# Kernel optimization log

Measured on AMD Instinct MI355X. Metric: run time of the kernel, lower is better.

## Reference

```python
import jax, jax.numpy as jnp
import numpy as np
import math


def _build_lookup(S):
    # Vectorized port of build_hierarchical_index_lookup_table (static, numpy).
    L = int(math.log2(S))
    total = 2 * S - 1
    max_valid = total - 2  # root is never a neighbor
    idx = np.full((S, L), -1, dtype=np.int32)
    cmask = np.zeros((S, L), dtype=bool)
    n = np.arange(S, dtype=np.int64)
    for lvl in range(L):
        if lvl == 0:
            nn = n ^ 1
            pair = n
        else:
            pair = n // 2 + S
            nn = pair ^ 1
        valid = nn <= max_valid
        idx[:, lvl] = np.where(valid, nn.astype(np.int32), idx[:, lvl])
        cmask[:, lvl] = np.where(valid, (pair < nn) & valid, cmask[:, lvl])
        n = nn
    return jnp.asarray(idx), jnp.asarray(cmask)


def _tree_kv(k, v, levels, scale):
    # Build parent nodes bottom-up. Parent K is the mean of its two children;
    # parent V is refined by the fused parent-self attention (build_parent_nodes):
    # 3-way softmax over [self, child0, child1] with eps 1e-9 in the denominator.
    K_parts, V_parts = [k], [v]
    Kc, Vc = k, v
    for _ in range(levels):
        Kc0, Kc1 = Kc[:, 0::2], Kc[:, 1::2]
        Vc0, Vc1 = Vc[:, 0::2], Vc[:, 1::2]
        Kp = 0.5 * (Kc0 + Kc1)
        Vp = 0.5 * (Vc0 + Vc1)
        s_self = jnp.einsum('bphd,bphd->bph', Kp, Kp) * scale
        s0 = jnp.einsum('bphd,bphd->bph', Kp, Kc0) * scale
        s1 = jnp.einsum('bphd,bphd->bph', Kp, Kc1) * scale
        m = jnp.maximum(s_self, jnp.maximum(s0, s1))
        e_self = jnp.exp(s_self - m)
        e0 = jnp.exp(s0 - m)
        e1 = jnp.exp(s1 - m)
        denom = e_self + e0 + e1 + 1e-9
        Vp = (e_self[..., None] * Vp + e0[..., None] * Vc0 + e1[..., None] * Vc1) / denom[..., None]
        K_parts.append(Kp)
        V_parts.append(Vp)
        Kc, Vc = Kp, Vp
    # Full tree: leaves first, then each parent level -> [B, 2S-1, H, D]
    return jnp.concatenate(K_parts, axis=1), jnp.concatenate(V_parts, axis=1)


def setup_inputs() -> dict:
    key = jax.random.key(0)
    kq, kk, kv = jax.random.split(key, 3)
    B, S, H, D = 4, 4096, 8, 64
    q = jax.random.normal(kq, (B, S, H, D), dtype=jnp.float32)
    k = jax.random.normal(kk, (B, S, H, D), dtype=jnp.float32)
    v = jax.random.normal(kv, (B, S, H, D), dtype=jnp.float32)
    return {'q': q, 'k': k, 'v': v}


def reference(q, k, v):
    B, S, H, D = q.shape
    L = int(math.log2(S))
    scale = 1.0 / math.sqrt(D)
    idx, cmask = _build_lookup(S)          # [S, L] int32, [S, L] bool
    Kf, Vf = _tree_kv(k, v, L, scale)      # [B, 2S-1, H, D]
    kc = Kf[:, idx]                        # [B, S, L, H, D] tree-indexed gather
    vc = Vf[:, idx]
    s_self = jnp.einsum('bshd,bshd->bsh', q, k) * scale
    s_cross = jnp.einsum('bshd,bslhd->bshl', q, kc) * scale
    s_cross = jnp.where(cmask[None, :, None, :], -jnp.inf, s_cross)
    m = jnp.maximum(s_self, jnp.max(s_cross, axis=-1))  # online-softmax max
    e_self = jnp.exp(s_self - m)
    e_cross = jnp.exp(s_cross - m[..., None])
    denom = e_self + jnp.sum(e_cross, axis=-1)
    out = (e_self[..., None] * v + jnp.einsum('bshl,bslhd->bshd', e_cross, vc)) / denom[..., None]
    return out
```

## Files before the change

### kernel.cpp

```cpp
#include <hip/hip_runtime.h>


#define S 4096
#define H 8
#define D 64
#define B 4
#define NINT 4094
#define NBH 32
#define SCALE 0.125f

__device__ inline float red16(float x) {
    x += __shfl_xor(x, 1);
    x += __shfl_xor(x, 2);
    x += __shfl_xor(x, 4);
    x += __shfl_xor(x, 8);
    return x;
}

__device__ inline float dot4(const float4 a, const float4 b) {
    return a.x * b.x + a.y * b.y + a.z * b.z + a.w * b.w;
}

__device__ inline void combine(const float4 k0, const float4 k1,
                               const float4 v0, const float4 v1,
                               float4& kp, float4& vp) {
    kp.x = 0.5f * (k0.x + k1.x);
    kp.y = 0.5f * (k0.y + k1.y);
    kp.z = 0.5f * (k0.z + k1.z);
    kp.w = 0.5f * (k0.w + k1.w);
    float pss = red16(dot4(kp, kp)) * SCALE;
    float p0  = red16(dot4(kp, k0)) * SCALE;
    float p1  = red16(dot4(kp, k1)) * SCALE;
    float m  = fmaxf(pss, fmaxf(p0, p1));
    float es = __expf(pss - m), e0 = __expf(p0 - m), e1 = __expf(p1 - m);
    float inv = 1.0f / (es + e0 + e1 + 1e-9f);
    float h = 0.5f * es;
    vp.x = ((h + e0) * v0.x + (h + e1) * v1.x) * inv;
    vp.y = ((h + e0) * v0.y + (h + e1) * v1.y) * inv;
    vp.z = ((h + e0) * v0.z + (h + e1) * v1.z) * inv;
    vp.w = ((h + e0) * v0.w + (h + e1) * v1.w) * inv;
}

__global__ __launch_bounds__(256) void tree_chunk(
    const float* __restrict__ k, const float* __restrict__ v,
    float* __restrict__ kt, float* __restrict__ vt)
{
    __shared__ float lk[127 * 64];
    __shared__ float lv[127 * 64];
    const int t = threadIdx.x;
    const int sub = t & 15;
    const int pg = t >> 4;
    const int blk = blockIdx.x;
    const int c = blk & 31;
    const int bh = blk >> 5;
    const int b = bh >> 3, h = bh & 7;

    for (int j = pg; j < 64; j += 16) {
        int s0 = c * 128 + 2 * j;
        size_t a0 = ((((size_t)b * S + s0) * H + h) * D) + sub * 4;
        float4 k0 = *(const float4*)(k + a0);
        float4 k1 = *(const float4*)(k + a0 + H * D);
        float4 v0 = *(const float4*)(v + a0);
        float4 v1 = *(const float4*)(v + a0 + H * D);
        float4 kp, vp;
        combine(k0, k1, v0, v1, kp, vp);
        *(float4*)(lk + j * 64 + sub * 4) = kp;
        *(float4*)(lv + j * 64 + sub * 4) = vp;
        size_t g = ((size_t)bh * NINT + c * 64 + j) * 64 + sub * 4;
        *(float4*)(kt + g) = kp;
        *(float4*)(vt + g) = vp;
    }
    __syncthreads();

    int coff = 0;
    for (int l = 2; l <= 7; ++l) {
        int np = 128 >> l;
        int poff = coff + (128 >> (l - 1));
        int goff = S - (S >> (l - 1));
        for (int j = pg; j < np; j += 16) {
            float4 k0 = *(const float4*)(lk + (coff + 2 * j) * 64 + sub * 4);
            float4 k1 = *(const float4*)(lk + (coff + 2 * j + 1) * 64 + sub * 4);
            float4 v0 = *(const float4*)(lv + (coff + 2 * j) * 64 + sub * 4);
            float4 v1 = *(const float4*)(lv + (coff + 2 * j + 1) * 64 + sub * 4);
            float4 kp, vp;
            combine(k0, k1, v0, v1, kp, vp);
            *(float4*)(lk + (poff + j) * 64 + sub * 4) = kp;
            *(float4*)(lv + (poff + j) * 64 + sub * 4) = vp;
            size_t g = ((size_t)bh * NINT + goff + c * np + j) * 64 + sub * 4;
            *(float4*)(kt + g) = kp;
            *(float4*)(vt + g) = vp;
        }
        __syncthreads();
        coff = poff;
    }
}

__global__ __launch_bounds__(256) void tree_top(
    float* __restrict__ kt, float* __restrict__ vt)
{
    __shared__ float lk[62 * 64];
    __shared__ float lv[62 * 64];
    const int t = threadIdx.x;
    const int sub = t & 15;
    const int pg = t >> 4;
    const int bh = blockIdx.x;

    for (int i = t; i < 512; i += 256) {
        size_t g = ((size_t)bh * NINT + (S - (S >> 6))) * 64 + i * 4;
        *(float4*)(lk + i * 4) = *(const float4*)(kt + g);
        *(float4*)(lv + i * 4) = *(const float4*)(vt + g);
    }
    __syncthreads();

    int coff = 0, cn = 32;
    for (int l = 8; l <= 11; ++l) {
        int np = cn >> 1;
        int poff = coff + cn;
        int goff = S - (S >> (l - 1));
        if (pg < np) {
            int j = pg;
            float4 k0 = *(const float4*)(lk + (coff + 2 * j) * 64 + sub * 4);
            float4 k1 = *(const float4*)(lk + (coff + 2 * j + 1) * 64 + sub * 4);
            float4 v0 = *(const float4*)(lv + (coff + 2 * j) * 64 + sub * 4);
            float4 v1 = *(const float4*)(lv + (coff + 2 * j + 1) * 64 + sub * 4);
            float4 kp, vp;
            combine(k0, k1, v0, v1, kp, vp);
            *(float4*)(lk + (poff + j) * 64 + sub * 4) = kp;
            *(float4*)(lv + (poff + j) * 64 + sub * 4) = vp;
            size_t g = ((size_t)bh * NINT + goff + j) * 64 + sub * 4;
            *(float4*)(kt + g) = kp;
            *(float4*)(vt + g) = vp;
        }
        __syncthreads();
        coff = poff; cn = np;
    }
}

__global__ __launch_bounds__(256) void attn(
    const float* __restrict__ q, const float* __restrict__ k,
    const float* __restrict__ v,
    const float* __restrict__ kt, const float* __restrict__ vt,
    float* __restrict__ out)
{
    int t = blockIdx.x * 256 + threadIdx.x;
    int lane = t & 63;
    int sub = lane & 15;
    int qi = lane >> 4;
    int w = t >> 6;
    int hg = w & 1;
    int s = (w >> 1) & (S - 1);
    int b = w >> 13;
    int h = hg * 4 + qi;
    int bh = b * 8 + h;
    size_t qa = ((((size_t)b * S + s) * H + h) * D) + sub * 4;

    float4 q4 = *(const float4*)(q + qa);
    float4 k4 = *(const float4*)(k + qa);
    float4 v4 = *(const float4*)(v + qa);
    float ss = red16(dot4(q4, k4)) * SCALE;

    float m = ss, denom = 1.0f;
    float4 acc = v4;
    size_t tb = (size_t)bh * NINT;

#pragma unroll
    for (int l = 0; l < 12; ++l) {
        if ((s >> l) & 1) {
            float4 kc, vc;
            if (l == 0) {
                kc = *(const float4*)(k + qa - H * D);
                vc = *(const float4*)(v + qa - H * D);
            } else {
                int node = (S - (S >> (l - 1))) + ((s >> l) ^ 1);
                size_t a = (tb + node) * 64 + sub * 4;
                kc = *(const float4*)(kt + a);
                vc = *(const float4*)(vt + a);
            }
            float sc = red16(dot4(q4, kc)) * SCALE;
            float nm = fmaxf(m, sc);
            float c1 = __expf(m - nm);
            float e  = __expf(sc - nm);
            denom = denom * c1 + e;
            acc.x = acc.x * c1 + e * vc.x;
            acc.y = acc.y * c1 + e * vc.y;
            acc.z = acc.z * c1 + e * vc.z;
            acc.w = acc.w * c1 + e * vc.w;
            m = nm;
        }
    }
    float inv = 1.0f / denom;
    float4 o;
    o.x = acc.x * inv; o.y = acc.y * inv; o.z = acc.z * inv; o.w = acc.w * inv;
    *(float4*)(out + qa) = o;
}

extern "C" void kernel_launch(void* const* d_in, const int* in_sizes, int n_in,
                              void* d_out, int out_size, void* d_ws, size_t ws_size,
                              hipStream_t stream) {
    const float* q = (const float*)d_in[0];
    const float* k = (const float*)d_in[1];
    const float* v = (const float*)d_in[2];
    float* outp = (float*)d_out;
    float* kt = (float*)d_ws;
    float* vt = kt + (size_t)NBH * NINT * D;

    hipLaunchKernelGGL(tree_chunk, dim3(NBH * 32), dim3(256), 0, stream,
                       k, v, kt, vt);
    hipLaunchKernelGGL(tree_top, dim3(NBH), dim3(256), 0, stream, kt, vt);
    hipLaunchKernelGGL(attn, dim3((B * S * 2 * 64) / 256), dim3(256), 0, stream,
                       q, k, v, kt, vt, outp);
}
```

Measured before the change: 181.2 us.

## Batch tree-node loads in attention and rebalance tree build across kernels

```diff
diff --git a/kernel.cpp b/kernel.cpp
--- a/kernel.cpp
+++ b/kernel.cpp
@@ -45,18 +45,20 @@
     const float* __restrict__ k, const float* __restrict__ v,
     float* __restrict__ kt, float* __restrict__ vt)
 {
-    __shared__ float lk[127 * 64];
-    __shared__ float lv[127 * 64];
+    __shared__ float lkA[32 * 64], lvA[32 * 64];
+    __shared__ float lkB[16 * 64], lvB[16 * 64];
     const int t = threadIdx.x;
     const int sub = t & 15;
     const int pg = t >> 4;
     const int blk = blockIdx.x;
-    const int c = blk & 31;
-    const int bh = blk >> 5;
+    const int c = blk & 63;
+    const int bh = blk >> 6;
     const int b = bh >> 3, h = bh & 7;
 
-    for (int j = pg; j < 64; j += 16) {
-        int s0 = c * 128 + 2 * j;
+#pragma unroll
+    for (int r = 0; r < 2; ++r) {
+        int j = pg + r * 16;
+        int s0 = c * 64 + 2 * j;
         size_t a0 = ((((size_t)b * S + s0) * H + h) * D) + sub * 4;
         float4 k0 = *(const float4*)(k + a0);
         float4 k1 = *(const float4*)(k + a0 + H * D);
@@ -64,75 +66,85 @@
         float4 v1 = *(const float4*)(v + a0 + H * D);
         float4 kp, vp;
         combine(k0, k1, v0, v1, kp, vp);
-        *(float4*)(lk + j * 64 + sub * 4) = kp;
-        *(float4*)(lv + j * 64 + sub * 4) = vp;
-        size_t g = ((size_t)bh * NINT + c * 64 + j) * 64 + sub * 4;
+        *(float4*)(lkA + j * 64 + sub * 4) = kp;
+        *(float4*)(lvA + j * 64 + sub * 4) = vp;
+        size_t g = ((size_t)bh * NINT + c * 32 + j) * 64 + sub * 4;
         *(float4*)(kt + g) = kp;
         *(float4*)(vt + g) = vp;
     }
     __syncthreads();
 
-    int coff = 0;
-    for (int l = 2; l <= 7; ++l) {
-        int np = 128 >> l;
-        int poff = coff + (128 >> (l - 1));
+    float *sk = lkA, *sv = lvA, *dk = lkB, *dv = lvB;
+#pragma unroll
+    for (int l = 2; l <= 6; ++l) {
+        int np = 64 >> l;
         int goff = S - (S >> (l - 1));
-        for (int j = pg; j < np; j += 16) {
-            float4 k0 = *(const float4*)(lk + (coff + 2 * j) * 64 + sub * 4);
-            float4 k1 = *(const float4*)(lk + (coff + 2 * j + 1) * 64 + sub * 4);
-            float4 v0 = *(const float4*)(lv + (coff + 2 * j) * 64 + sub * 4);
-            float4 v1 = *(const float4*)(lv + (coff + 2 * j + 1) * 64 + sub * 4);
+        if (pg < np) {
+            int j = pg;
+            float4 k0 = *(const float4*)(sk + (2 * j) * 64 + sub * 4);
+            float4 k1 = *(const float4*)(sk + (2 * j + 1) * 64 + sub * 4);
+            float4 v0 = *(const float4*)(sv + (2 * j) * 64 + sub * 4);
+            float4 v1 = *(const float4*)(sv + (2 * j + 1) * 64 + sub * 4);
             float4 kp, vp;
             combine(k0, k1, v0, v1, kp, vp);
-            *(float4*)(lk + (poff + j) * 64 + sub * 4) = kp;
-            *(float4*)(lv + (poff + j) * 64 + sub * 4) = vp;
+            if (l < 6) {
+                *(float4*)(dk + j * 64 + sub * 4) = kp;
+                *(float4*)(dv + j * 64 + sub * 4) = vp;
+            }
             size_t g = ((size_t)bh * NINT + goff + c * np + j) * 64 + sub * 4;
             *(float4*)(kt + g) = kp;
             *(float4*)(vt + g) = vp;
         }
         __syncthreads();
-        coff = poff;
+        float* tp;
+        tp = sk; sk = dk; dk = tp;
+        tp = sv; sv = dv; dv = tp;
     }
 }
 
 __global__ __launch_bounds__(256) void tree_top(
     float* __restrict__ kt, float* __restrict__ vt)
 {
-    __shared__ float lk[62 * 64];
-    __shared__ float lv[62 * 64];
+    __shared__ float lkA[64 * 64], lvA[64 * 64];
+    __shared__ float lkB[32 * 64], lvB[32 * 64];
     const int t = threadIdx.x;
     const int sub = t & 15;
     const int pg = t >> 4;
     const int bh = blockIdx.x;
 
-    for (int i = t; i < 512; i += 256) {
-        size_t g = ((size_t)bh * NINT + (S - (S >> 6))) * 64 + i * 4;
-        *(float4*)(lk + i * 4) = *(const float4*)(kt + g);
-        *(float4*)(lv + i * 4) = *(const float4*)(vt + g);
+    for (int i = t; i < 1024; i += 256) {
+        size_t g = ((size_t)bh * NINT + 3968) * 64 + i * 4;
+        *(float4*)(lkA + i * 4) = *(const float4*)(kt + g);
+        *(float4*)(lvA + i * 4) = *(const float4*)(vt + g);
     }
     __syncthreads();
 
-    int coff = 0, cn = 32;
-    for (int l = 8; l <= 11; ++l) {
+    float *sk = lkA, *sv = lvA, *dk = lkB, *dv = lvB;
+    int cn = 64;
+#pragma unroll
+    for (int l = 7; l <= 11; ++l) {
         int np = cn >> 1;
-        int poff = coff + cn;
         int goff = S - (S >> (l - 1));
-        if (pg < np) {
-            int j = pg;
-            float4 k0 = *(const float4*)(lk + (coff + 2 * j) * 64 + sub * 4);
-            float4 k1 = *(const float4*)(lk + (coff + 2 * j + 1) * 64 + sub * 4);
-            float4 v0 = *(const float4*)(lv + (coff + 2 * j) * 64 + sub * 4);
-            float4 v1 = *(const float4*)(lv + (coff + 2 * j + 1) * 64 + sub * 4);
+        for (int j = pg; j < np; j += 16) {
+            float4 k0 = *(const float4*)(sk + (2 * j) * 64 + sub * 4);
+            float4 k1 = *(const float4*)(sk + (2 * j + 1) * 64 + sub * 4);
+            float4 v0 = *(const float4*)(sv + (2 * j) * 64 + sub * 4);
+            float4 v1 = *(const float4*)(sv + (2 * j + 1) * 64 + sub * 4);
             float4 kp, vp;
             combine(k0, k1, v0, v1, kp, vp);
-            *(float4*)(lk + (poff + j) * 64 + sub * 4) = kp;
-            *(float4*)(lv + (poff + j) * 64 + sub * 4) = vp;
+            if (l < 11) {
+                *(float4*)(dk + j * 64 + sub * 4) = kp;
+                *(float4*)(dv + j * 64 + sub * 4) = vp;
+            }
             size_t g = ((size_t)bh * NINT + goff + j) * 64 + sub * 4;
             *(float4*)(kt + g) = kp;
             *(float4*)(vt + g) = vp;
         }
         __syncthreads();
-        coff = poff; cn = np;
+        float* tp;
+        tp = sk; sk = dk; dk = tp;
+        tp = sv; sv = dv; dv = tp;
+        cn = np;
     }
 }
 
@@ -157,35 +169,49 @@
     float4 q4 = *(const float4*)(q + qa);
     float4 k4 = *(const float4*)(k + qa);
     float4 v4 = *(const float4*)(v + qa);
-    float ss = red16(dot4(q4, k4)) * SCALE;
-
-    float m = ss, denom = 1.0f;
-    float4 acc = v4;
+
+    float4 kc[12], vc[12];
     size_t tb = (size_t)bh * NINT;
-
 #pragma unroll
     for (int l = 0; l < 12; ++l) {
         if ((s >> l) & 1) {
-            float4 kc, vc;
             if (l == 0) {
-                kc = *(const float4*)(k + qa - H * D);
-                vc = *(const float4*)(v + qa - H * D);
+                kc[0] = *(const float4*)(k + qa - H * D);
+                vc[0] = *(const float4*)(v + qa - H * D);
             } else {
                 int node = (S - (S >> (l - 1))) + ((s >> l) ^ 1);
                 size_t a = (tb + node) * 64 + sub * 4;
-                kc = *(const float4*)(kt + a);
-                vc = *(const float4*)(vt + a);
+                kc[l] = *(const float4*)(kt + a);
+                vc[l] = *(const float4*)(vt + a);
             }
-            float sc = red16(dot4(q4, kc)) * SCALE;
-            float nm = fmaxf(m, sc);
-            float c1 = __expf(m - nm);
-            float e  = __expf(sc - nm);
-            denom = denom * c1 + e;
-            acc.x = acc.x * c1 + e * vc.x;
-            acc.y = acc.y * c1 + e * vc.y;
-            acc.z = acc.z * c1 + e * vc.z;
-            acc.w = acc.w * c1 + e * vc.w;
-            m = nm;
+        }
+    }
+
+    float ss = red16(dot4(q4, k4)) * SCALE;
+    float sc[12];
+#pragma unroll
+    for (int l = 0; l < 12; ++l) {
+        if ((s >> l) & 1) sc[l] = red16(dot4(q4, kc[l])) * SCALE;
+        else              sc[l] = -1e38f;
+    }
+
+    float m = ss;
+#pragma unroll
+    for (int l = 0; l < 12; ++l) m = fmaxf(m, sc[l]);
+
+    float es = __expf(ss - m);
+    float denom = es;
+    float4 acc;
+    acc.x = es * v4.x; acc.y = es * v4.y; acc.z = es * v4.z; acc.w = es * v4.w;
+#pragma unroll
+    for (int l = 0; l < 12; ++l) {
+        if ((s >> l) & 1) {
+            float e = __expf(sc[l] - m);
+            denom += e;
+            acc.x += e * vc[l].x;
+            acc.y += e * vc[l].y;
+            acc.z += e * vc[l].z;
+            acc.w += e * vc[l].w;
         }
     }
     float inv = 1.0f / denom;
@@ -204,7 +230,7 @@
     float* kt = (float*)d_ws;
     float* vt = kt + (size_t)NBH * NINT * D;
 
-    hipLaunchKernelGGL(tree_chunk, dim3(NBH * 32), dim3(256), 0, stream,
+    hipLaunchKernelGGL(tree_chunk, dim3(NBH * 64), dim3(256), 0, stream,
                        k, v, kt, vt);
     hipLaunchKernelGGL(tree_top, dim3(NBH), dim3(256), 0, stream, kt, vt);
     hipLaunchKernelGGL(attn, dim3((B * S * 2 * 64) / 256), dim3(256), 0, stream,
```

Result: faster. 175.7 us (-3.0%).
